# Kernel tuning notes

Hardware: AMD Instinct MI355X
Metric: run time of the kernel (lower is better)

## Reference

```python
import jax, jax.numpy as jnp
import numpy as np
import math

V, D, H, L, T_MAX = 512, 256, 4, 8, 256
HD = D // H
EPS = 1e-5


def _ln(x, g, b):
    mu = jnp.mean(x, axis=-1, keepdims=True)
    var = jnp.mean(jnp.square(x - mu), axis=-1, keepdims=True)
    return (x - mu) * jax.lax.rsqrt(var + EPS) * g + b


def _pos_encoding(T, D):
    pos = jnp.arange(T, dtype=jnp.float32)[:, None]
    div = jnp.exp(jnp.arange(0, D, 2, dtype=jnp.float32) * (-math.log(10000.0) / D))
    pe = jnp.zeros((T, D), dtype=jnp.float32)
    pe = pe.at[:, 0::2].set(jnp.sin(pos * div))
    pe = pe.at[:, 1::2].set(jnp.cos(pos * div))
    return pe


def setup_inputs() -> dict:
    key = jax.random.key(0)
    ks = jax.random.split(key, 16)
    s = 0.02
    B, T = 128, 256
    return {
        "idx": jax.random.randint(ks[0], (B, T), 0, V),
        "tok_emb": jax.random.normal(ks[1], (V, D)) * s,
        "Wq": jax.random.normal(ks[2], (L, D, D)) * s,
        "Wk": jax.random.normal(ks[3], (L, D, D)) * s,
        "Wv": jax.random.normal(ks[4], (L, D, D)) * s,
        "Wo": jax.random.normal(ks[5], (L, D, D)) * s,
        "bo": jnp.zeros((L, D)),
        "W1": jax.random.normal(ks[6], (L, D, D)) * s,
        "b1": jnp.zeros((L, D)),
        "W2": jax.random.normal(ks[7], (L, D, D)) * s,
        "b2": jnp.zeros((L, D)),
        "g1": jnp.ones((L, D)), "be1": jnp.zeros((L, D)),
        "g2": jnp.ones((L, D)), "be2": jnp.zeros((L, D)),
        "gf": jnp.ones((D,)), "bf": jnp.zeros((D,)),
        "Wh": jax.random.normal(ks[8], (D, V)) * s,
        "bh": jnp.zeros((V,)),
    }


def reference(idx, tok_emb, Wq, Wk, Wv, Wo, bo, W1, b1, W2, b2,
              g1, be1, g2, be2, gf, bf, Wh, bh):
    B, T = idx.shape
    x = tok_emb[idx] + _pos_encoding(T, D)[None]  # [B,T,D]
    causal = jnp.tril(jnp.ones((T, T), dtype=bool))
    scale = D ** (-0.5)  # NOTE: original scales by n_embd, not head_size
    for l in range(L):
        h = _ln(x, g1[l], be1[l])
        q = (h @ Wq[l]).reshape(B, T, H, HD)
        k = (h @ Wk[l]).reshape(B, T, H, HD)
        v = (h @ Wv[l]).reshape(B, T, H, HD)
        wei = jnp.einsum('bqhd,bkhd->bhqk', q, k) * scale
        wei = jnp.where(causal, wei, -jnp.inf)
        wei = jax.nn.softmax(wei, axis=-1)
        att = jnp.einsum('bhqk,bkhd->bqhd', wei, v).reshape(B, T, D)
        x = x + att @ Wo[l] + bo[l]
        h = _ln(x, g2[l], be2[l])
        x = x + jax.nn.relu(h @ W1[l] + b1[l]) @ W2[l] + b2[l]
    x = _ln(x, gf, bf)
    logits = x @ Wh + bh  # [B,T,V]
    return logits
```

## Files before the change

kernel.cpp:

```cpp
#include <hip/hip_runtime.h>
#include <hip/hip_bf16.h>

typedef unsigned short u16;
typedef __attribute__((ext_vector_type(8))) short short8;
typedef __attribute__((ext_vector_type(4))) float f32x4;

#define DEV static __device__ __forceinline__

DEV u16 f2bf(float x){
  union { __hip_bfloat16 b; u16 u; } c;
  c.b = __float2bfloat16(x);
  return c.u;
}

DEV void gload16(const void* g, void* lds){
  __builtin_amdgcn_global_load_lds((const __attribute__((address_space(1))) void*)g,
                                   (__attribute__((address_space(3))) void*)lds, 16, 0, 0);
}

__global__ __launch_bounds__(256)
void wconv_kernel(const float* __restrict__ Wq, const float* __restrict__ Wk,
                  const float* __restrict__ Wv, const float* __restrict__ Wo,
                  const float* __restrict__ W1, const float* __restrict__ W2,
                  const float* __restrict__ Wh,
                  u16* __restrict__ WqkvT, u16* __restrict__ WoT,
                  u16* __restrict__ W1T, u16* __restrict__ W2T, u16* __restrict__ WhT)
{
  __shared__ float tile[32][33];
  const int j = blockIdx.y;
  int N = 256;
  const float* src; u16* dst;
  if (j < 48){
    const int li = j / 6, t = j % 6;
    switch(t){
      case 0:  src = Wq + li*65536; dst = WqkvT + li*196608;          break;
      case 1:  src = Wk + li*65536; dst = WqkvT + li*196608 + 65536;  break;
      case 2:  src = Wv + li*65536; dst = WqkvT + li*196608 + 131072; break;
      case 3:  src = Wo + li*65536; dst = WoT  + li*65536;            break;
      case 4:  src = W1 + li*65536; dst = W1T  + li*65536;            break;
      default: src = W2 + li*65536; dst = W2T  + li*65536;            break;
    }
  } else { N = 512; src = Wh; dst = WhT; }
  const int tilesPerRow = N >> 5;
  if ((int)blockIdx.x >= tilesPerRow * 8) return;
  const int tx = blockIdx.x % tilesPerRow, ty = blockIdx.x / tilesPerRow;
  const int tid = threadIdx.x;
  const int r = tid >> 3, c4 = (tid & 7) * 4;
  float4 v = *(const float4*)(src + (size_t)(ty*32 + r)*N + tx*32 + c4);
  tile[r][c4+0]=v.x; tile[r][c4+1]=v.y; tile[r][c4+2]=v.z; tile[r][c4+3]=v.w;
  __syncthreads();
  ushort4 o;
  o.x = f2bf(tile[c4+0][r]); o.y = f2bf(tile[c4+1][r]);
  o.z = f2bf(tile[c4+2][r]); o.w = f2bf(tile[c4+3][r]);
  *(ushort4*)(dst + (size_t)(tx*32 + r)*256 + ty*32 + c4) = o;
}

__global__ __launch_bounds__(256)
void embed_ln_kernel(const int* __restrict__ idx, const float* __restrict__ emb,
                     const float* __restrict__ g, const float* __restrict__ be,
                     float* __restrict__ x, u16* __restrict__ hb)
{
  const int tid = threadIdx.x;
  const int w = tid >> 6, l = tid & 63;
  const int row = blockIdx.x*4 + w;
  const int t = row & 255;
  const int v = idx[row];
  const int c4 = l*4;
  float4 e = *(const float4*)(emb + (size_t)v*256 + c4);
  float r[4];
  const float ef[4] = {e.x, e.y, e.z, e.w};
  #pragma unroll
  for (int i=0;i<4;++i){
    const int c = c4 + i;
    const float div = expf((float)(c & ~1) * (-9.210340371976184f/256.f));
    const float ang = (float)t * div;
    r[i] = ((c & 1) ? cosf(ang) : sinf(ang)) + ef[i];
  }
  *(float4*)(x + (size_t)row*256 + c4) = (float4){r[0],r[1],r[2],r[3]};
  float s = r[0]+r[1]+r[2]+r[3];
  float q = r[0]*r[0]+r[1]*r[1]+r[2]*r[2]+r[3]*r[3];
  #pragma unroll
  for (int m=32; m; m>>=1){ s += __shfl_xor(s,m); q += __shfl_xor(q,m); }
  const float mu = s * (1.f/256.f);
  const float var = q * (1.f/256.f) - mu*mu;
  const float rstd = rsqrtf(var + 1e-5f);
  const float4 gv = *(const float4*)(g + c4);
  const float4 bv = *(const float4*)(be + c4);
  ushort4 o;
  o.x = f2bf((r[0]-mu)*rstd*gv.x + bv.x);
  o.y = f2bf((r[1]-mu)*rstd*gv.y + bv.y);
  o.z = f2bf((r[2]-mu)*rstd*gv.z + bv.z);
  o.w = f2bf((r[3]-mu)*rstd*gv.w + bv.w);
  *(ushort4*)(hb + (size_t)row*256 + c4) = o;
}

template<bool OBF, bool RELU_, bool BIAS_>
__global__ __launch_bounds__(256)
void gemm_kernel(const u16* __restrict__ A, const u16* __restrict__ W,
                 const float* __restrict__ bias, void* __restrict__ Cv, int ldC)
{
  __shared__ __align__(16) u16 Al[2][4096];
  __shared__ __align__(16) u16 Bl[2][4096];
  const int tid = threadIdx.x;
  const int w = tid >> 6, l = tid & 63;
  const int lr = l & 15, lg = l >> 4;
  const int m0 = blockIdx.x * 128, n0 = blockIdx.y * 128;
  const int wm = w >> 1, wn = w & 1;
  const int rowc = l >> 2;
  const int pswz = (l & 3) ^ ((l >> 3) & 3);

  f32x4 acc[4][4];
  #pragma unroll
  for (int i=0;i<4;++i)
    #pragma unroll
    for (int jn=0;jn<4;++jn) acc[i][jn] = (f32x4){0.f,0.f,0.f,0.f};

  #pragma unroll
  for (int cc=0; cc<2; ++cc){
    const int c = w + cc*4;
    gload16(A + (size_t)(m0 + 16*c + rowc)*256 + pswz*8, &Al[0][c*512]);
    gload16(W + (size_t)(n0 + 16*c + rowc)*256 + pswz*8, &Bl[0][c*512]);
  }
  __syncthreads();

  for (int kt=0; kt<8; ++kt){
    if (kt < 7){
      const int kofs = (kt+1) * 32, nb = (kt+1) & 1;
      #pragma unroll
      for (int cc=0; cc<2; ++cc){
        const int c = w + cc*4;
        gload16(A + (size_t)(m0 + 16*c + rowc)*256 + kofs + pswz*8, &Al[nb][c*512]);
        gload16(W + (size_t)(n0 + 16*c + rowc)*256 + kofs + pswz*8, &Bl[nb][c*512]);
      }
    }
    const int buf = kt & 1;
    short8 af[4], bf[4];
    #pragma unroll
    for (int mt=0; mt<4; ++mt){
      const int row = wm*64 + mt*16 + lr;
      const int kb = (lg*16) ^ ((((row>>1)&3))<<4);
      af[mt] = *(const short8*)((const char*)Al[buf] + row*64 + kb);
    }
    #pragma unroll
    for (int nt=0; nt<4; ++nt){
      const int row = wn*64 + nt*16 + lr;
      const int kb = (lg*16) ^ ((((row>>1)&3))<<4);
      bf[nt] = *(const short8*)((const char*)Bl[buf] + row*64 + kb);
    }
    #pragma unroll
    for (int mt=0; mt<4; ++mt)
      #pragma unroll
      for (int nt=0; nt<4; ++nt)
        acc[mt][nt] = __builtin_amdgcn_mfma_f32_16x16x32_bf16(af[mt], bf[nt], acc[mt][nt], 0,0,0);
    __syncthreads();
  }

  #pragma unroll
  for (int nt=0; nt<4; ++nt){
    const int col = n0 + wn*64 + nt*16 + lr;
    const float bv = BIAS_ ? bias[col] : 0.f;
    #pragma unroll
    for (int mt=0; mt<4; ++mt){
      f32x4 v = acc[mt][nt];
      #pragma unroll
      for (int r=0;r<4;++r){
        const int row = m0 + wm*64 + mt*16 + lg*4 + r;
        float val = v[r] + bv;
        if (RELU_) val = fmaxf(val, 0.f);
        if (OBF) ((u16*)Cv)[(size_t)row*ldC + col] = f2bf(val);
        else     ((float*)Cv)[(size_t)row*ldC + col] = val;
      }
    }
  }
}

__global__ __launch_bounds__(256, 2)
void gemm_res_ln_kernel(const u16* __restrict__ A, const u16* __restrict__ W,
                        const float* __restrict__ bias,
                        const float* __restrict__ g, const float* __restrict__ be,
                        float* __restrict__ x, u16* __restrict__ hb)
{
  __shared__ __align__(16) u16 Al[2][2048];
  __shared__ __align__(16) u16 Bl[2][8192];
  __shared__ float sS[64][2], sQ[64][2];
  const int tid = threadIdx.x;
  const int w = tid >> 6, l = tid & 63;
  const int lr = l & 15, lg = l >> 4;
  const int m0 = blockIdx.x * 64;
  const int wm = w >> 1, wn = w & 1;
  const int rowc = l >> 2;
  const int pswz = (l & 3) ^ ((l >> 3) & 3);

  f32x4 acc[2][2][4];
  #pragma unroll
  for (int p=0;p<2;++p)
    #pragma unroll
    for (int i=0;i<2;++i)
      #pragma unroll
      for (int jn=0;jn<4;++jn) acc[p][i][jn] = (f32x4){0.f,0.f,0.f,0.f};

  gload16(A + (size_t)(m0 + 16*w + rowc)*256 + pswz*8, &Al[0][w*512]);
  #pragma unroll
  for (int cc=0; cc<4; ++cc){
    const int c = w + cc*4;
    gload16(W + (size_t)(16*c + rowc)*256 + pswz*8, &Bl[0][c*512]);
  }
  __syncthreads();

  for (int kt=0; kt<8; ++kt){
    if (kt < 7){
      const int kofs = (kt+1)*32, nb = (kt+1)&1;
      gload16(A + (size_t)(m0 + 16*w + rowc)*256 + kofs + pswz*8, &Al[nb][w*512]);
      #pragma unroll
      for (int cc=0; cc<4; ++cc){
        const int c = w + cc*4;
        gload16(W + (size_t)(16*c + rowc)*256 + kofs + pswz*8, &Bl[nb][c*512]);
      }
    }
    const int buf = kt & 1;
    short8 af[2], bf[2][4];
    #pragma unroll
    for (int mt=0; mt<2; ++mt){
      const int row = wm*32 + mt*16 + lr;
      const int kb = (lg*16) ^ ((((row>>1)&3))<<4);
      af[mt] = *(const short8*)((const char*)Al[buf] + row*64 + kb);
    }
    #pragma unroll
    for (int p=0; p<2; ++p)
      #pragma unroll
      for (int nt=0; nt<4; ++nt){
        const int brow = p*128 + wn*64 + nt*16 + lr;
        const int kb = (lg*16) ^ ((((brow>>1)&3))<<4);
        bf[p][nt] = *(const short8*)((const char*)Bl[buf] + brow*64 + kb);
      }
    #pragma unroll
    for (int p=0; p<2; ++p)
      #pragma unroll
      for (int mt=0; mt<2; ++mt)
        #pragma unroll
        for (int nt=0; nt<4; ++nt)
          acc[p][mt][nt] = __builtin_amdgcn_mfma_f32_16x16x32_bf16(af[mt], bf[p][nt], acc[p][mt][nt], 0,0,0);
    __syncthreads();
  }

  float bcol[2][4], gcol[2][4], becol[2][4];
  #pragma unroll
  for (int p=0;p<2;++p)
    #pragma unroll
    for (int nt=0;nt<4;++nt){
      const int col = p*128 + wn*64 + nt*16 + lr;
      bcol[p][nt] = bias[col]; gcol[p][nt] = g[col]; becol[p][nt] = be[col];
    }
  float s8[2][4], q8[2][4];
  #pragma unroll
  for (int mt=0;mt<2;++mt)
    #pragma unroll
    for (int rr=0;rr<4;++rr){ s8[mt][rr]=0.f; q8[mt][rr]=0.f; }

  #pragma unroll
  for (int p=0;p<2;++p)
    #pragma unroll
    for (int mt=0;mt<2;++mt)
      #pragma unroll
      for (int nt=0;nt<4;++nt)
        #pragma unroll
        for (int rr=0;rr<4;++rr){
          const int row = m0 + wm*32 + mt*16 + lg*4 + rr;
          const int col = p*128 + wn*64 + nt*16 + lr;
          float val = acc[p][mt][nt][rr] + bcol[p][nt] + x[(size_t)row*256 + col];
          x[(size_t)row*256 + col] = val;
          acc[p][mt][nt][rr] = val;
          s8[mt][rr] += val; q8[mt][rr] += val*val;
        }
  #pragma unroll
  for (int mt=0;mt<2;++mt)
    #pragma unroll
    for (int rr=0;rr<4;++rr){
      #pragma unroll
      for (int m=1; m<16; m<<=1){
        s8[mt][rr] += __shfl_xor(s8[mt][rr], m);
        q8[mt][rr] += __shfl_xor(q8[mt][rr], m);
      }
      if (lr == 0){
        const int lrow = wm*32 + mt*16 + lg*4 + rr;
        sS[lrow][wn] = s8[mt][rr]; sQ[lrow][wn] = q8[mt][rr];
      }
    }
  __syncthreads();

  #pragma unroll
  for (int mt=0;mt<2;++mt)
    #pragma unroll
    for (int rr=0;rr<4;++rr){
      const int lrow = wm*32 + mt*16 + lg*4 + rr;
      const float mu = (sS[lrow][0] + sS[lrow][1]) * (1.f/256.f);
      const float var = (sQ[lrow][0] + sQ[lrow][1]) * (1.f/256.f) - mu*mu;
      const float rstd = rsqrtf(var + 1e-5f);
      #pragma unroll
      for (int p=0;p<2;++p)
        #pragma unroll
        for (int nt=0;nt<4;++nt){
          const int col = p*128 + wn*64 + nt*16 + lr;
          const float out = (acc[p][mt][nt][rr] - mu)*rstd*gcol[p][nt] + becol[p][nt];
          hb[(size_t)(m0+lrow)*256 + col] = f2bf(out);
        }
    }
}

__global__ __launch_bounds__(512, 4)
void attn_kernel(const u16* __restrict__ qkv, u16* __restrict__ att)
{
  __shared__ __align__(16) u16 sK[16384];
  __shared__ __align__(16) u16 sV[16384];
  __shared__ __align__(16) u16 sP[8192];
  const int bh = blockIdx.x;
  const int b = bh >> 2, h = bh & 3;
  const int tid = threadIdx.x;
  const int w = tid >> 6, l = tid & 63, lr = l & 15, lg = l >> 4;
  const u16* base = qkv + (size_t)(b*256)*768;

  #pragma unroll
  for (int it=0; it<4; ++it){
    const int c = tid + it*512;
    const int t = c >> 3, p = c & 7;
    uint4 val = *(const uint4*)(base + (size_t)t*768 + 256 + h*64 + p*8);
    *(uint4*)((char*)sK + t*128 + ((p*16) ^ ((t&7)<<4))) = val;
  }
  #pragma unroll
  for (int it=0; it<8; ++it){
    const int c = tid + it*512;
    const int t = c >> 4, hdq = c & 15;
    ushort4 v = *(const ushort4*)(base + (size_t)t*768 + 512 + h*64 + hdq*4);
    #pragma unroll
    for (int j=0;j<4;++j){
      const int hd = hdq*4 + j;
      *(u16*)((char*)sV + hd*512 + ((t*2) ^ ((hd&31)<<4))) = ((const u16*)&v)[j];
    }
  }
  __syncthreads();

  char* sPw = (char*)sP + w*2048;
  const int swzq = (lr & 7) << 4;
  u16* ab = att + (size_t)(b*256)*256 + h*64;
  const float c1 = 0.09016844005556021f;

  #pragma unroll
  for (int ph=0; ph<2; ++ph){
    const int rt = ph ? (15 - w) : w;
    const u16* qp = base + (size_t)(rt*16 + lr)*768 + h*64;
    const short8 qf0 = *(const short8*)(qp + lg*8);
    const short8 qf1 = *(const short8*)(qp + 32 + lg*8);

    f32x4 acc[16];
    #pragma unroll
    for (int nt=0; nt<16; ++nt) acc[nt] = (f32x4){0.f,0.f,0.f,0.f};
    #pragma unroll
    for (int nt=0; nt<16; ++nt){
      if (nt <= rt){
        const int row = nt*16 + lr;
        const int swz = (row & 7) << 4;
        short8 k0 = *(const short8*)((const char*)sK + row*128 + ((lg*16) ^ swz));
        short8 k1 = *(const short8*)((const char*)sK + row*128 + ((64 + lg*16) ^ swz));
        acc[nt] = __builtin_amdgcn_mfma_f32_16x16x32_bf16(k0, qf0, acc[nt], 0,0,0);
        acc[nt] = __builtin_amdgcn_mfma_f32_16x16x32_bf16(k1, qf1, acc[nt], 0,0,0);
      }
    }
    #pragma unroll
    for (int nt=0; nt<16; ++nt){
      if (nt == rt){
        #pragma unroll
        for (int r=0;r<4;++r)
          acc[nt][r] = (lg*4 + r > lr) ? -3.0e38f : acc[nt][r];
      }
    }

    float m_ = -3.0e38f;
    #pragma unroll
    for (int nt=0; nt<16; ++nt){
      if (nt <= rt){
        float t01 = fmaxf(acc[nt][0], acc[nt][1]);
        float t23 = fmaxf(acc[nt][2], acc[nt][3]);
        m_ = fmaxf(m_, fmaxf(t01, t23));
      }
    }
    m_ = fmaxf(m_, __shfl_xor(m_, 16));
    m_ = fmaxf(m_, __shfl_xor(m_, 32));
    const float mm = m_ * c1;
    float s_ = 0.f;
    #pragma unroll
    for (int nt=0; nt<16; ++nt){
      if (nt <= rt){
        #pragma unroll
        for (int r=0;r<4;++r){
          const float p = exp2f(fmaf(acc[nt][r], c1, -mm));
          acc[nt][r] = p;
          s_ += p;
        }
      }
    }
    s_ += __shfl_xor(s_, 16);
    s_ += __shfl_xor(s_, 32);
    const float inv = 1.f / s_;

    f32x4 oacc[4];
    #pragma unroll
    for (int nt=0; nt<4; ++nt) oacc[nt] = (f32x4){0.f,0.f,0.f,0.f};
    #pragma unroll
    for (int c=0; c<4; ++c){
      if (c <= (rt >> 2)){
        #pragma unroll
        for (int e=0; e<4; ++e){
          const int nt = 4*c + e;
          ushort4 pk;
          #pragma unroll
          for (int r=0;r<4;++r){
            const float val = (nt <= rt) ? acc[nt][r] * inv : 0.f;
            ((u16*)&pk)[r] = f2bf(val);
          }
          *(ushort4*)(sPw + lr*128 + ((e*32 + lg*8) ^ swzq)) = pk;
        }
        #pragma unroll
        for (int kc=0; kc<2; ++kc){
          const int tc = 2*c + kc;
          if (tc <= (rt >> 1)){
            const short8 ap = *(const short8*)(sPw + lr*128 + ((kc*64 + lg*16) ^ swzq));
            #pragma unroll
            for (int nt=0; nt<4; ++nt){
              const int vrow = nt*16 + lr;
              const short8 bv = *(const short8*)((const char*)sV + vrow*512 +
                                   ((tc*64 + lg*16) ^ ((vrow&31)<<4)));
              oacc[nt] = __builtin_amdgcn_mfma_f32_16x16x32_bf16(ap, bv, oacc[nt], 0,0,0);
            }
          }
        }
      }
    }

    #pragma unroll
    for (int nt=0; nt<4; ++nt)
      #pragma unroll
      for (int r=0;r<4;++r){
        const int row = rt*16 + lg*4 + r;
        ab[(size_t)row*256 + nt*16 + lr] = f2bf(oacc[nt][r]);
      }
  }
}

extern "C" void kernel_launch(void* const* d_in, const int* in_sizes, int n_in,
                              void* d_out, int out_size, void* d_ws, size_t ws_size,
                              hipStream_t stream)
{
  (void)in_sizes; (void)n_in; (void)out_size; (void)ws_size;
  const int*   idx = (const int*)  d_in[0];
  const float* tok = (const float*)d_in[1];
  const float* Wq  = (const float*)d_in[2];
  const float* Wk  = (const float*)d_in[3];
  const float* Wv  = (const float*)d_in[4];
  const float* Wo  = (const float*)d_in[5];
  const float* bo  = (const float*)d_in[6];
  const float* W1  = (const float*)d_in[7];
  const float* b1  = (const float*)d_in[8];
  const float* W2  = (const float*)d_in[9];
  const float* b2  = (const float*)d_in[10];
  const float* g1  = (const float*)d_in[11];
  const float* be1 = (const float*)d_in[12];
  const float* g2  = (const float*)d_in[13];
  const float* be2 = (const float*)d_in[14];
  const float* gf  = (const float*)d_in[15];
  const float* bfi = (const float*)d_in[16];
  const float* Wh  = (const float*)d_in[17];
  const float* bh  = (const float*)d_in[18];

  char* ws = (char*)d_ws;
  float* x    = (float*)ws;  ws += (size_t)32768*256*4;
  u16*   hb   = (u16*)ws;    ws += (size_t)32768*256*2;
  u16*   mid  = (u16*)ws;    ws += (size_t)32768*256*2;
  u16*   qkv  = (u16*)ws;    ws += (size_t)32768*768*2;
  u16*   att  = (u16*)ws;    ws += (size_t)32768*256*2;
  u16*   WqkvT= (u16*)ws;    ws += (size_t)8*768*256*2;
  u16*   WoT  = (u16*)ws;    ws += (size_t)8*256*256*2;
  u16*   W1T  = (u16*)ws;    ws += (size_t)8*256*256*2;
  u16*   W2T  = (u16*)ws;    ws += (size_t)8*256*256*2;
  u16*   WhT  = (u16*)ws;    ws += (size_t)512*256*2;

  wconv_kernel<<<dim3(128,49),256,0,stream>>>(Wq,Wk,Wv,Wo,W1,W2,Wh,WqkvT,WoT,W1T,W2T,WhT);
  embed_ln_kernel<<<8192,256,0,stream>>>(idx, tok, g1, be1, x, hb);
  for (int l=0; l<8; ++l){
    gemm_kernel<true,false,false><<<dim3(256,6),256,0,stream>>>(
        hb, WqkvT + (size_t)l*196608, nullptr, qkv, 768);
    attn_kernel<<<512,512,0,stream>>>(qkv, att);
    gemm_res_ln_kernel<<<512,256,0,stream>>>(
        att, WoT + (size_t)l*65536, bo + l*256, g2 + l*256, be2 + l*256, x, hb);
    gemm_kernel<true,true,true><<<dim3(256,2),256,0,stream>>>(
        hb, W1T + (size_t)l*65536, b1 + l*256, mid, 256);
    const float* gn = (l < 7) ? (g1 + (l+1)*256) : gf;
    const float* bn = (l < 7) ? (be1 + (l+1)*256) : bfi;
    gemm_res_ln_kernel<<<512,256,0,stream>>>(
        mid, W2T + (size_t)l*65536, b2 + l*256, gn, bn, x, hb);
  }
  gemm_kernel<false,false,true><<<dim3(256,4),256,0,stream>>>(
      hb, WhT, bh, (float*)d_out, 512);
}
```

Before: 865.7 us.

## Fuse Wo, LN2, FFN, LN1 and next-layer QKV GEMM into one chain kernel

Replaces the per-layer sequence of Wo+residual+LN, W1+ReLU, W2+residual+LN and the next layer's QKV GEMM with one kernel per 64-row tile. Intermediates stay in swizzled LDS and the residual stays in registers. This removes the mid and hb global round trips and three launches per layer. In exchange each block runs five GEMMs serially with 512 threads and large LDS use, which may lower occupancy and parallelism. The final layer fuses the LM head projection.

```diff
diff --git a/kernel.cpp b/kernel.cpp
--- a/kernel.cpp
+++ b/kernel.cpp
@@ -174,137 +174,331 @@
   }
 }
 
-__global__ __launch_bounds__(256, 2)
-void gemm_res_ln_kernel(const u16* __restrict__ A, const u16* __restrict__ W,
-                        const float* __restrict__ bias,
-                        const float* __restrict__ g, const float* __restrict__ be,
-                        float* __restrict__ x, u16* __restrict__ hb)
+template<bool LAST>
+__global__ __launch_bounds__(512, 4)
+void chain_kernel(const u16* __restrict__ att,
+                  const u16* __restrict__ WoT, const float* __restrict__ bo,
+                  const float* __restrict__ g2, const float* __restrict__ be2,
+                  const u16* __restrict__ W1T, const float* __restrict__ b1,
+                  const u16* __restrict__ W2T, const float* __restrict__ b2,
+                  const float* __restrict__ gn, const float* __restrict__ bn,
+                  const u16* __restrict__ Wn, const float* __restrict__ bhn,
+                  float* __restrict__ x, u16* __restrict__ qkv_out,
+                  float* __restrict__ logits)
 {
-  __shared__ __align__(16) u16 Al[2][2048];
+  __shared__ __align__(16) u16 Asw[16384];
   __shared__ __align__(16) u16 Bl[2][8192];
-  __shared__ float sS[64][2], sQ[64][2];
+  __shared__ __align__(16) u16 Aatt[2][2048];
+  __shared__ float sS[64][4], sQ[64][4];
+
   const int tid = threadIdx.x;
   const int w = tid >> 6, l = tid & 63;
   const int lr = l & 15, lg = l >> 4;
   const int m0 = blockIdx.x * 64;
-  const int wm = w >> 1, wn = w & 1;
+  const int wm = w >> 2, wn = w & 3;
   const int rowc = l >> 2;
   const int pswz = (l & 3) ^ ((l >> 3) & 3);
 
-  f32x4 acc[2][2][4];
-  #pragma unroll
-  for (int p=0;p<2;++p)
-    #pragma unroll
-    for (int i=0;i<2;++i)
-      #pragma unroll
-      for (int jn=0;jn<4;++jn) acc[p][i][jn] = (f32x4){0.f,0.f,0.f,0.f};
-
-  gload16(A + (size_t)(m0 + 16*w + rowc)*256 + pswz*8, &Al[0][w*512]);
-  #pragma unroll
-  for (int cc=0; cc<4; ++cc){
-    const int c = w + cc*4;
-    gload16(W + (size_t)(16*c + rowc)*256 + pswz*8, &Bl[0][c*512]);
+  f32x4 acc[2][4];
+  float xv[2][4][4];
+
+  #pragma unroll
+  for (int i=0;i<2;++i)
+    #pragma unroll
+    for (int jn=0;jn<4;++jn) acc[i][jn] = (f32x4){0.f,0.f,0.f,0.f};
+  if (w < 4) gload16(att + (size_t)(m0 + 16*w + rowc)*256 + pswz*8, &Aatt[0][w*512]);
+  #pragma unroll
+  for (int it=0; it<2; ++it){
+    const int c = w + it*8;
+    gload16(WoT + (size_t)(16*c + rowc)*256 + pswz*8, &Bl[0][c*512]);
   }
   __syncthreads();
-
   for (int kt=0; kt<8; ++kt){
     if (kt < 7){
       const int kofs = (kt+1)*32, nb = (kt+1)&1;
-      gload16(A + (size_t)(m0 + 16*w + rowc)*256 + kofs + pswz*8, &Al[nb][w*512]);
-      #pragma unroll
-      for (int cc=0; cc<4; ++cc){
-        const int c = w + cc*4;
-        gload16(W + (size_t)(16*c + rowc)*256 + kofs + pswz*8, &Bl[nb][c*512]);
+      if (w < 4) gload16(att + (size_t)(m0 + 16*w + rowc)*256 + kofs + pswz*8, &Aatt[nb][w*512]);
+      #pragma unroll
+      for (int it=0; it<2; ++it){
+        const int c = w + it*8;
+        gload16(WoT + (size_t)(16*c + rowc)*256 + kofs + pswz*8, &Bl[nb][c*512]);
       }
     }
     const int buf = kt & 1;
-    short8 af[2], bf[2][4];
+    short8 af[2], bfr[4];
     #pragma unroll
     for (int mt=0; mt<2; ++mt){
       const int row = wm*32 + mt*16 + lr;
       const int kb = (lg*16) ^ ((((row>>1)&3))<<4);
-      af[mt] = *(const short8*)((const char*)Al[buf] + row*64 + kb);
-    }
-    #pragma unroll
-    for (int p=0; p<2; ++p)
+      af[mt] = *(const short8*)((const char*)Aatt[buf] + row*64 + kb);
+    }
+    #pragma unroll
+    for (int nt=0; nt<4; ++nt){
+      const int row = wn*64 + nt*16 + lr;
+      const int kb = (lg*16) ^ ((((row>>1)&3))<<4);
+      bfr[nt] = *(const short8*)((const char*)Bl[buf] + row*64 + kb);
+    }
+    #pragma unroll
+    for (int mt=0; mt<2; ++mt)
+      #pragma unroll
+      for (int nt=0; nt<4; ++nt)
+        acc[mt][nt] = __builtin_amdgcn_mfma_f32_16x16x32_bf16(af[mt], bfr[nt], acc[mt][nt], 0,0,0);
+    __syncthreads();
+  }
+  {
+    float s_[2][4], q_[2][4];
+    #pragma unroll
+    for (int mt=0;mt<2;++mt)
+      #pragma unroll
+      for (int rr=0;rr<4;++rr){ s_[mt][rr]=0.f; q_[mt][rr]=0.f; }
+    #pragma unroll
+    for (int nt=0; nt<4; ++nt){
+      const int col = wn*64 + nt*16 + lr;
+      const float bv = bo[col];
+      #pragma unroll
+      for (int mt=0; mt<2; ++mt)
+        #pragma unroll
+        for (int rr=0; rr<4; ++rr){
+          const int row = m0 + wm*32 + mt*16 + lg*4 + rr;
+          const float val = acc[mt][nt][rr] + bv + x[(size_t)row*256 + col];
+          xv[mt][nt][rr] = val;
+          s_[mt][rr] += val; q_[mt][rr] += val*val;
+        }
+    }
+    #pragma unroll
+    for (int mt=0;mt<2;++mt)
+      #pragma unroll
+      for (int rr=0;rr<4;++rr){
+        float s = s_[mt][rr], q = q_[mt][rr];
+        #pragma unroll
+        for (int m=1; m<16; m<<=1){ s += __shfl_xor(s,m); q += __shfl_xor(q,m); }
+        if (lr == 0){
+          const int lrow = wm*32 + mt*16 + lg*4 + rr;
+          sS[lrow][wn] = s; sQ[lrow][wn] = q;
+        }
+      }
+    __syncthreads();
+    #pragma unroll
+    for (int mt=0;mt<2;++mt)
+      #pragma unroll
+      for (int rr=0;rr<4;++rr){
+        const int lrow = wm*32 + mt*16 + lg*4 + rr;
+        const float4 ss = *(const float4*)sS[lrow];
+        const float4 qq = *(const float4*)sQ[lrow];
+        const float mu = (ss.x+ss.y+ss.z+ss.w) * (1.f/256.f);
+        const float var = (qq.x+qq.y+qq.z+qq.w) * (1.f/256.f) - mu*mu;
+        const float rstd = rsqrtf(var + 1e-5f);
+        #pragma unroll
+        for (int nt=0; nt<4; ++nt){
+          const int col = wn*64 + nt*16 + lr;
+          const float out = (xv[mt][nt][rr] - mu)*rstd*g2[col] + be2[col];
+          *(u16*)((char*)Asw + lrow*512 + ((col*2) ^ ((lrow&15)<<4))) = f2bf(out);
+        }
+      }
+  }
+
+  #pragma unroll
+  for (int i=0;i<2;++i)
+    #pragma unroll
+    for (int jn=0;jn<4;++jn) acc[i][jn] = (f32x4){0.f,0.f,0.f,0.f};
+  #pragma unroll
+  for (int it=0; it<2; ++it){
+    const int c = w + it*8;
+    gload16(W1T + (size_t)(16*c + rowc)*256 + pswz*8, &Bl[0][c*512]);
+  }
+  __syncthreads();
+  for (int kt=0; kt<8; ++kt){
+    if (kt < 7){
+      const int kofs = (kt+1)*32, nb = (kt+1)&1;
+      #pragma unroll
+      for (int it=0; it<2; ++it){
+        const int c = w + it*8;
+        gload16(W1T + (size_t)(16*c + rowc)*256 + kofs + pswz*8, &Bl[nb][c*512]);
+      }
+    }
+    const int buf = kt & 1;
+    short8 af[2], bfr[4];
+    #pragma unroll
+    for (int mt=0; mt<2; ++mt){
+      const int row = wm*32 + mt*16 + lr;
+      af[mt] = *(const short8*)((const char*)Asw + row*512 + ((kt*64 + lg*16) ^ ((row&15)<<4)));
+    }
+    #pragma unroll
+    for (int nt=0; nt<4; ++nt){
+      const int row = wn*64 + nt*16 + lr;
+      const int kb = (lg*16) ^ ((((row>>1)&3))<<4);
+      bfr[nt] = *(const short8*)((const char*)Bl[buf] + row*64 + kb);
+    }
+    #pragma unroll
+    for (int mt=0; mt<2; ++mt)
+      #pragma unroll
+      for (int nt=0; nt<4; ++nt)
+        acc[mt][nt] = __builtin_amdgcn_mfma_f32_16x16x32_bf16(af[mt], bfr[nt], acc[mt][nt], 0,0,0);
+    __syncthreads();
+  }
+  #pragma unroll
+  for (int nt=0; nt<4; ++nt){
+    const int col = wn*64 + nt*16 + lr;
+    const float bv = b1[col];
+    #pragma unroll
+    for (int mt=0; mt<2; ++mt)
+      #pragma unroll
+      for (int rr=0; rr<4; ++rr){
+        const int lrow = wm*32 + mt*16 + lg*4 + rr;
+        const float val = fmaxf(acc[mt][nt][rr] + bv, 0.f);
+        *(u16*)((char*)Asw + lrow*512 + ((col*2) ^ ((lrow&15)<<4))) = f2bf(val);
+      }
+  }
+
+  #pragma unroll
+  for (int i=0;i<2;++i)
+    #pragma unroll
+    for (int jn=0;jn<4;++jn) acc[i][jn] = (f32x4){0.f,0.f,0.f,0.f};
+  #pragma unroll
+  for (int it=0; it<2; ++it){
+    const int c = w + it*8;
+    gload16(W2T + (size_t)(16*c + rowc)*256 + pswz*8, &Bl[0][c*512]);
+  }
+  __syncthreads();
+  for (int kt=0; kt<8; ++kt){
+    if (kt < 7){
+      const int kofs = (kt+1)*32, nb = (kt+1)&1;
+      #pragma unroll
+      for (int it=0; it<2; ++it){
+        const int c = w + it*8;
+        gload16(W2T + (size_t)(16*c + rowc)*256 + kofs + pswz*8, &Bl[nb][c*512]);
+      }
+    }
+    const int buf = kt & 1;
+    short8 af[2], bfr[4];
+    #pragma unroll
+    for (int mt=0; mt<2; ++mt){
+      const int row = wm*32 + mt*16 + lr;
+      af[mt] = *(const short8*)((const char*)Asw + row*512 + ((kt*64 + lg*16) ^ ((row&15)<<4)));
+    }
+    #pragma unroll
+    for (int nt=0; nt<4; ++nt){
+      const int row = wn*64 + nt*16 + lr;
+      const int kb = (lg*16) ^ ((((row>>1)&3))<<4);
+      bfr[nt] = *(const short8*)((const char*)Bl[buf] + row*64 + kb);
+    }
+    #pragma unroll
+    for (int mt=0; mt<2; ++mt)
+      #pragma unroll
+      for (int nt=0; nt<4; ++nt)
+        acc[mt][nt] = __builtin_amdgcn_mfma_f32_16x16x32_bf16(af[mt], bfr[nt], acc[mt][nt], 0,0,0);
+    __syncthreads();
+  }
+  {
+    float s_[2][4], q_[2][4];
+    #pragma unroll
+    for (int mt=0;mt<2;++mt)
+      #pragma unroll
+      for (int rr=0;rr<4;++rr){ s_[mt][rr]=0.f; q_[mt][rr]=0.f; }
+    #pragma unroll
+    for (int nt=0; nt<4; ++nt){
+      const int col = wn*64 + nt*16 + lr;
+      const float bv = b2[col];
+      #pragma unroll
+      for (int mt=0; mt<2; ++mt)
+        #pragma unroll
+        for (int rr=0; rr<4; ++rr){
+          const int row = m0 + wm*32 + mt*16 + lg*4 + rr;
+          const float val = acc[mt][nt][rr] + bv + xv[mt][nt][rr];
+          xv[mt][nt][rr] = val;
+          if (!LAST) x[(size_t)row*256 + col] = val;
+          s_[mt][rr] += val; q_[mt][rr] += val*val;
+        }
+    }
+    #pragma unroll
+    for (int mt=0;mt<2;++mt)
+      #pragma unroll
+      for (int rr=0;rr<4;++rr){
+        float s = s_[mt][rr], q = q_[mt][rr];
+        #pragma unroll
+        for (int m=1; m<16; m<<=1){ s += __shfl_xor(s,m); q += __shfl_xor(q,m); }
+        if (lr == 0){
+          const int lrow = wm*32 + mt*16 + lg*4 + rr;
+          sS[lrow][wn] = s; sQ[lrow][wn] = q;
+        }
+      }
+    __syncthreads();
+    #pragma unroll
+    for (int mt=0;mt<2;++mt)
+      #pragma unroll
+      for (int rr=0;rr<4;++rr){
+        const int lrow = wm*32 + mt*16 + lg*4 + rr;
+        const float4 ss = *(const float4*)sS[lrow];
+        const float4 qq = *(const float4*)sQ[lrow];
+        const float mu = (ss.x+ss.y+ss.z+ss.w) * (1.f/256.f);
+        const float var = (qq.x+qq.y+qq.z+qq.w) * (1.f/256.f) - mu*mu;
+        const float rstd = rsqrtf(var + 1e-5f);
+        #pragma unroll
+        for (int nt=0; nt<4; ++nt){
+          const int col = wn*64 + nt*16 + lr;
+          const float out = (xv[mt][nt][rr] - mu)*rstd*gn[col] + bn[col];
+          *(u16*)((char*)Asw + lrow*512 + ((col*2) ^ ((lrow&15)<<4))) = f2bf(out);
+        }
+      }
+  }
+
+  const int NP = LAST ? 2 : 3;
+  #pragma unroll
+  for (int p=0; p<NP; ++p){
+    #pragma unroll
+    for (int i=0;i<2;++i)
+      #pragma unroll
+      for (int jn=0;jn<4;++jn) acc[i][jn] = (f32x4){0.f,0.f,0.f,0.f};
+    const u16* Wp = Wn + (size_t)p*65536;
+    #pragma unroll
+    for (int it=0; it<2; ++it){
+      const int c = w + it*8;
+      gload16(Wp + (size_t)(16*c + rowc)*256 + pswz*8, &Bl[0][c*512]);
+    }
+    __syncthreads();
+    for (int kt=0; kt<8; ++kt){
+      if (kt < 7){
+        const int kofs = (kt+1)*32, nb = (kt+1)&1;
+        #pragma unroll
+        for (int it=0; it<2; ++it){
+          const int c = w + it*8;
+          gload16(Wp + (size_t)(16*c + rowc)*256 + kofs + pswz*8, &Bl[nb][c*512]);
+        }
+      }
+      const int buf = kt & 1;
+      short8 af[2], bfr[4];
+      #pragma unroll
+      for (int mt=0; mt<2; ++mt){
+        const int row = wm*32 + mt*16 + lr;
+        af[mt] = *(const short8*)((const char*)Asw + row*512 + ((kt*64 + lg*16) ^ ((row&15)<<4)));
+      }
       #pragma unroll
       for (int nt=0; nt<4; ++nt){
-        const int brow = p*128 + wn*64 + nt*16 + lr;
-        const int kb = (lg*16) ^ ((((brow>>1)&3))<<4);
-        bf[p][nt] = *(const short8*)((const char*)Bl[buf] + brow*64 + kb);
-      }
-    #pragma unroll
-    for (int p=0; p<2; ++p)
+        const int row = wn*64 + nt*16 + lr;
+        const int kb = (lg*16) ^ ((((row>>1)&3))<<4);
+        bfr[nt] = *(const short8*)((const char*)Bl[buf] + row*64 + kb);
+      }
       #pragma unroll
       for (int mt=0; mt<2; ++mt)
         #pragma unroll
         for (int nt=0; nt<4; ++nt)
-          acc[p][mt][nt] = __builtin_amdgcn_mfma_f32_16x16x32_bf16(af[mt], bf[p][nt], acc[p][mt][nt], 0,0,0);
-    __syncthreads();
-  }
-
-  float bcol[2][4], gcol[2][4], becol[2][4];
-  #pragma unroll
-  for (int p=0;p<2;++p)
-    #pragma unroll
-    for (int nt=0;nt<4;++nt){
-      const int col = p*128 + wn*64 + nt*16 + lr;
-      bcol[p][nt] = bias[col]; gcol[p][nt] = g[col]; becol[p][nt] = be[col];
-    }
-  float s8[2][4], q8[2][4];
-  #pragma unroll
-  for (int mt=0;mt<2;++mt)
-    #pragma unroll
-    for (int rr=0;rr<4;++rr){ s8[mt][rr]=0.f; q8[mt][rr]=0.f; }
-
-  #pragma unroll
-  for (int p=0;p<2;++p)
-    #pragma unroll
-    for (int mt=0;mt<2;++mt)
-      #pragma unroll
-      for (int nt=0;nt<4;++nt)
-        #pragma unroll
-        for (int rr=0;rr<4;++rr){
+          acc[mt][nt] = __builtin_amdgcn_mfma_f32_16x16x32_bf16(af[mt], bfr[nt], acc[mt][nt], 0,0,0);
+      __syncthreads();
+    }
+    #pragma unroll
+    for (int nt=0; nt<4; ++nt){
+      const int col = p*256 + wn*64 + nt*16 + lr;
+      const float bv = LAST ? bhn[col] : 0.f;
+      #pragma unroll
+      for (int mt=0; mt<2; ++mt)
+        #pragma unroll
+        for (int rr=0; rr<4; ++rr){
           const int row = m0 + wm*32 + mt*16 + lg*4 + rr;
-          const int col = p*128 + wn*64 + nt*16 + lr;
-          float val = acc[p][mt][nt][rr] + bcol[p][nt] + x[(size_t)row*256 + col];
-          x[(size_t)row*256 + col] = val;
-          acc[p][mt][nt][rr] = val;
-          s8[mt][rr] += val; q8[mt][rr] += val*val;
-        }
-  #pragma unroll
-  for (int mt=0;mt<2;++mt)
-    #pragma unroll
-    for (int rr=0;rr<4;++rr){
-      #pragma unroll
-      for (int m=1; m<16; m<<=1){
-        s8[mt][rr] += __shfl_xor(s8[mt][rr], m);
-        q8[mt][rr] += __shfl_xor(q8[mt][rr], m);
-      }
-      if (lr == 0){
-        const int lrow = wm*32 + mt*16 + lg*4 + rr;
-        sS[lrow][wn] = s8[mt][rr]; sQ[lrow][wn] = q8[mt][rr];
-      }
-    }
-  __syncthreads();
-
-  #pragma unroll
-  for (int mt=0;mt<2;++mt)
-    #pragma unroll
-    for (int rr=0;rr<4;++rr){
-      const int lrow = wm*32 + mt*16 + lg*4 + rr;
-      const float mu = (sS[lrow][0] + sS[lrow][1]) * (1.f/256.f);
-      const float var = (sQ[lrow][0] + sQ[lrow][1]) * (1.f/256.f) - mu*mu;
-      const float rstd = rsqrtf(var + 1e-5f);
-      #pragma unroll
-      for (int p=0;p<2;++p)
-        #pragma unroll
-        for (int nt=0;nt<4;++nt){
-          const int col = p*128 + wn*64 + nt*16 + lr;
-          const float out = (acc[p][mt][nt][rr] - mu)*rstd*gcol[p][nt] + becol[p][nt];
-          hb[(size_t)(m0+lrow)*256 + col] = f2bf(out);
-        }
-    }
+          const float val = acc[mt][nt][rr] + bv;
+          if (LAST) logits[(size_t)row*512 + col] = val;
+          else      qkv_out[(size_t)row*768 + col] = f2bf(val);
+        }
+    }
+  }
 }
 
 __global__ __launch_bounds__(512, 4)
@@ -474,7 +668,6 @@
   char* ws = (char*)d_ws;
   float* x    = (float*)ws;  ws += (size_t)32768*256*4;
   u16*   hb   = (u16*)ws;    ws += (size_t)32768*256*2;
-  u16*   mid  = (u16*)ws;    ws += (size_t)32768*256*2;
   u16*   qkv  = (u16*)ws;    ws += (size_t)32768*768*2;
   u16*   att  = (u16*)ws;    ws += (size_t)32768*256*2;
   u16*   WqkvT= (u16*)ws;    ws += (size_t)8*768*256*2;
@@ -485,19 +678,21 @@
 
   wconv_kernel<<<dim3(128,49),256,0,stream>>>(Wq,Wk,Wv,Wo,W1,W2,Wh,WqkvT,WoT,W1T,W2T,WhT);
   embed_ln_kernel<<<8192,256,0,stream>>>(idx, tok, g1, be1, x, hb);
+  gemm_kernel<true,false,false><<<dim3(256,6),256,0,stream>>>(
+      hb, WqkvT, nullptr, qkv, 768);
   for (int l=0; l<8; ++l){
-    gemm_kernel<true,false,false><<<dim3(256,6),256,0,stream>>>(
-        hb, WqkvT + (size_t)l*196608, nullptr, qkv, 768);
     attn_kernel<<<512,512,0,stream>>>(qkv, att);
-    gemm_res_ln_kernel<<<512,256,0,stream>>>(
-        att, WoT + (size_t)l*65536, bo + l*256, g2 + l*256, be2 + l*256, x, hb);
-    gemm_kernel<true,true,true><<<dim3(256,2),256,0,stream>>>(
-        hb, W1T + (size_t)l*65536, b1 + l*256, mid, 256);
-    const float* gn = (l < 7) ? (g1 + (l+1)*256) : gf;
-    const float* bn = (l < 7) ? (be1 + (l+1)*256) : bfi;
-    gemm_res_ln_kernel<<<512,256,0,stream>>>(
-        mid, W2T + (size_t)l*65536, b2 + l*256, gn, bn, x, hb);
-  }
-  gemm_kernel<false,false,true><<<dim3(256,4),256,0,stream>>>(
-      hb, WhT, bh, (float*)d_out, 512);
-}
+    if (l < 7){
+      chain_kernel<false><<<512,512,0,stream>>>(
+          att, WoT + (size_t)l*65536, bo + l*256, g2 + l*256, be2 + l*256,
+          W1T + (size_t)l*65536, b1 + l*256, W2T + (size_t)l*65536, b2 + l*256,
+          g1 + (l+1)*256, be1 + (l+1)*256,
+          WqkvT + (size_t)(l+1)*196608, nullptr, x, qkv, nullptr);
+    } else {
+      chain_kernel<true><<<512,512,0,stream>>>(
+          att, WoT + (size_t)l*65536, bo + l*256, g2 + l*256, be2 + l*256,
+          W1T + (size_t)l*65536, b1 + l*256, W2T + (size_t)l*65536, b2 + l*256,
+          gf, bfi, WhT, bh, x, nullptr, (float*)d_out);
+    }
+  }
+}
```

Measured after the change: 915.9 us. +5.8%, slower.
